# Kernel optimization log

Hardware: AMD Instinct MI355X
Metric: run time of the kernel (lower is better)

The kernel has to match this reference:

```python
import jax, jax.numpy as jnp
import numpy as np

DIM = 128          # per-stream channels (init arg `dim`)
C = 2 * DIM        # fused channels
NH = 8             # num_heads
HD = C // NH       # head_dim = 32
K = 3              # kernel_size
DIL = (2, 3)       # dilation list
ND = len(DIL)
SCALE = HD ** -0.5


def setup_inputs() -> dict:
    key = jax.random.key(0)
    ks = jax.random.split(key, 4)
    B, H, W = 4, 80, 80
    rgb = jax.random.normal(ks[0], (B, DIM, H, W), jnp.float32)
    ir = jax.random.normal(ks[1], (B, DIM, H, W), jnp.float32)
    w_qkv = jax.random.normal(ks[2], (3 * C, C), jnp.float32) * (C ** -0.5)
    w_proj = jax.random.normal(ks[3], (C, C), jnp.float32) * (C ** -0.5)
    b_proj = jnp.zeros((C,), jnp.float32)
    return {"rgb": rgb, "ir": ir, "w_qkv": w_qkv, "w_proj": w_proj, "b_proj": b_proj}


def _unfold(x, k, d):
    # nn.Unfold(k, dilation=d, padding=d*(k-1)//2, stride=1) -> [B, c, k*k, H, W]
    B, c, H, W = x.shape
    p = d * (k - 1) // 2
    xp = jnp.pad(x, ((0, 0), (0, 0), (p, p), (p, p)))
    pats = [xp[:, :, i * d:i * d + H, j * d:j * d + W]
            for i in range(k) for j in range(k)]
    return jnp.stack(pats, axis=2)


def _dilate_attention(q, k, v, d):
    # q,k,v: [B, c, H, W] with c = C // ND; attention over k*k dilated neighborhood
    B, c, H, W = q.shape
    h = c // HD
    N = H * W
    qr = q.reshape(B, h, HD, N)                      # [B,h,hd,N]
    ku = _unfold(k, K, d).reshape(B, h, HD, K * K, N)  # [B,h,hd,K2,N]
    vu = _unfold(v, K, d).reshape(B, h, HD, K * K, N)
    attn = jnp.einsum('bhdn,bhdkn->bhnk', qr, ku) * SCALE   # [B,h,N,K2]
    attn = jax.nn.softmax(attn, axis=-1)
    out = jnp.einsum('bhnk,bhdkn->bnhd', attn, vu)          # head-major channels
    return out.reshape(B, H, W, c)


def reference(rgb, ir, w_qkv, w_proj, b_proj):
    y = jnp.concatenate([rgb, ir], axis=1)            # [B, C, H, W]
    B, Cc, H, W = y.shape
    # 1x1 conv qkv, then split channels as [3, num_dilation, C//num_dilation]
    qkv = jnp.einsum('bchw,oc->bohw', y, w_qkv).reshape(B, 3, ND, Cc // ND, H, W)
    outs = [_dilate_attention(qkv[:, 0, i], qkv[:, 1, i], qkv[:, 2, i], DIL[i])
            for i in range(ND)]
    x = jnp.concatenate(outs, axis=-1)                # [B, H, W, C], dilation-major
    x = x @ w_proj.T + b_proj                         # proj Linear(C, C)
    # residual: add rgb to first half of channels, ir to second half
    return x + y.transpose(0, 2, 3, 1)
```

## Files before the change

kernel.cpp:

```cpp
#include <hip/hip_runtime.h>

#define HH 80
#define WW 80
#define NPIX 6400
#define NB 4
#define BN 25600
#define CDIM 256
#define QKVC 768
#define SCALE 0.17677669529663689f

typedef __attribute__((ext_vector_type(8))) short short8;
typedef __attribute__((ext_vector_type(4))) float floatx4;

__device__ __forceinline__ float b2f(ushort u) {
    return __uint_as_float(((uint)u) << 16);
}
__device__ __forceinline__ ushort f2b(float f) {
    uint u = __float_as_uint(f);
    return (ushort)((u + 0x7fffu + ((u >> 16) & 1u)) >> 16);
}
__device__ __forceinline__ void unpack8(uint4 v, float* f) {
    f[0] = __uint_as_float(v.x << 16); f[1] = __uint_as_float(v.x & 0xffff0000u);
    f[2] = __uint_as_float(v.y << 16); f[3] = __uint_as_float(v.y & 0xffff0000u);
    f[4] = __uint_as_float(v.z << 16); f[5] = __uint_as_float(v.z & 0xffff0000u);
    f[6] = __uint_as_float(v.w << 16); f[7] = __uint_as_float(v.w & 0xffff0000u);
}
__device__ __forceinline__ void gload_lds16(const void* gptr, void* lptr) {
    __builtin_amdgcn_global_load_lds(
        (const __attribute__((address_space(1))) unsigned int*)gptr,
        (__attribute__((address_space(3))) unsigned int*)lptr,
        16, 0, 0);
}

__global__ __launch_bounds__(256) void cast_w_k(
    const float* __restrict__ wq, const float* __restrict__ wp,
    ushort* __restrict__ wqb, ushort* __restrict__ wpb)
{
    int i = blockIdx.x * 256 + threadIdx.x;
    if (i < QKVC * CDIM) wqb[i] = f2b(wq[i]);
    if (i < CDIM * CDIM) wpb[i] = f2b(wp[i]);
}

__global__ __launch_bounds__(256) void cast_y_k(
    const float* __restrict__ rgb, const float* __restrict__ ir,
    ushort* __restrict__ Yb)
{
    __shared__ ushort T[32][72];
    const int tid = threadIdx.x;
    const int pix0 = blockIdx.x * 64;
    const int cb = blockIdx.y;
    const int b = blockIdx.z;

    const int pl = tid & 63, cg = tid >> 6;
    #pragma unroll
    for (int cc = 0; cc < 32; cc += 4) {
        int c = cb * 32 + cc + cg;
        const float* src = (c < 128) ? (rgb + ((size_t)b * 128 + c) * NPIX)
                                     : (ir + ((size_t)b * 128 + (c - 128)) * NPIX);
        T[cc + cg][pl] = f2b(src[pix0 + pl]);
    }
    __syncthreads();
    const int nl = tid >> 2, c0 = (tid & 3) * 8;
    ushort tmp[8];
    #pragma unroll
    for (int j = 0; j < 8; ++j) tmp[j] = T[c0 + j][nl];
    uint4 v;
    v.x = tmp[0] | ((uint)tmp[1] << 16);
    v.y = tmp[2] | ((uint)tmp[3] << 16);
    v.z = tmp[4] | ((uint)tmp[5] << 16);
    v.w = tmp[6] | ((uint)tmp[7] << 16);
    *(uint4*)(&Yb[((size_t)(b * NPIX + pix0 + nl)) * CDIM + cb * 32 + c0]) = v;
}

__global__ __launch_bounds__(256) void gemm_qkv_mfma(
    const ushort* __restrict__ Yb, const ushort* __restrict__ Wb,
    ushort* __restrict__ qkvb)
{
    __shared__ __align__(16) ushort As[128 * 40];
    __shared__ __align__(16) ushort Bs[128 * 40];
    const int tid = threadIdx.x;
    const int lane = tid & 63;
    const int wave = tid >> 6;
    const int wr = wave >> 1, wc = wave & 1;
    const int l15 = lane & 15, quad = lane >> 4;
    const int n0 = blockIdx.x * 128;
    const int o0 = blockIdx.y * 128;

    const int sm = tid >> 2;
    const int sk = (tid & 3) * 8;

    floatx4 acc[4][4] = {};

    for (int k0 = 0; k0 < CDIM; k0 += 32) {
        #pragma unroll
        for (int p = 0; p < 2; ++p) {
            int m = sm + p * 64;
            *(uint4*)(&As[m * 40 + sk]) =
                *(const uint4*)(&Yb[(size_t)(n0 + m) * CDIM + k0 + sk]);
            *(uint4*)(&Bs[m * 40 + sk]) =
                *(const uint4*)(&Wb[(size_t)(o0 + m) * CDIM + k0 + sk]);
        }
        __syncthreads();
        short8 af[4], bfr[4];
        #pragma unroll
        for (int i = 0; i < 4; ++i)
            af[i] = *(const short8*)(&As[(wr * 64 + i * 16 + l15) * 40 + quad * 8]);
        #pragma unroll
        for (int j = 0; j < 4; ++j)
            bfr[j] = *(const short8*)(&Bs[(wc * 64 + j * 16 + l15) * 40 + quad * 8]);
        #pragma unroll
        for (int i = 0; i < 4; ++i)
            #pragma unroll
            for (int j = 0; j < 4; ++j)
                acc[i][j] = __builtin_amdgcn_mfma_f32_16x16x32_bf16(
                    af[i], bfr[j], acc[i][j], 0, 0, 0);
        __syncthreads();
    }
    #pragma unroll
    for (int i = 0; i < 4; ++i)
        #pragma unroll
        for (int j = 0; j < 4; ++j)
            #pragma unroll
            for (int r = 0; r < 4; ++r) {
                int n = n0 + wr * 64 + i * 16 + quad * 4 + r;
                int o = o0 + wc * 64 + j * 16 + l15;
                qkvb[(size_t)n * QKVC + o] = f2b(acc[i][j][r]);
            }
}

template<int D>
__device__ __forceinline__ void attn_tile(
    const ushort* __restrict__ qkvb, ushort* __restrict__ Xb,
    ushort* kl, ushort* vl, int b, int dil_i, int head, int y0, int x0)
{
    constexpr int RW = 16 + 2 * D;
    constexpr int RP = RW * RW;
    const int tid = threadIdx.x;
    const int lane = tid & 63;
    const int wave = tid >> 6;
    const int obase = dil_i * 128 + head * 32;

    const int px = tid & 15, py = tid >> 4;
    const int n = b * NPIX + (y0 + py) * WW + (x0 + px);
    float q[32];
    {
        const uint4* qp = (const uint4*)(qkvb + (size_t)n * QKVC + obase);
        uint4 v0 = qp[0], v1 = qp[1], v2 = qp[2], v3 = qp[3];
        unpack8(v0, q); unpack8(v1, q + 8); unpack8(v2, q + 16); unpack8(v3, q + 24);
    }

    for (int p0 = 0; p0 < RP; p0 += 64) {
        int p = p0 + lane;
        int ry = p / RW, rx = p % RW;
        int gy = min(max(y0 - D + ry, 0), HH - 1);
        int gx = min(max(x0 - D + rx, 0), WW - 1);
        const ushort* row = qkvb + (size_t)(b * NPIX + gy * WW + gx) * QKVC + obase + wave * 8;
        if (p < RP) {
            gload_lds16(row + 256, kl + (size_t)(wave * RP + p0) * 8);
            gload_lds16(row + 512, vl + (size_t)(wave * RP + p0) * 8);
        }
    }
    __syncthreads();

    float sc[9];
    #pragma unroll
    for (int t = 0; t < 9; ++t) {
        const int dy = t / 3 - 1, dx = t % 3 - 1;
        const int yy = y0 + py + dy * D, xx = x0 + px + dx * D;
        const int p = (py + D + dy * D) * RW + (px + D + dx * D);
        float s = 0.f;
        if (yy >= 0 && yy < HH && xx >= 0 && xx < WW) {
            #pragma unroll
            for (int c = 0; c < 4; ++c) {
                float kv[8];
                unpack8(*(const uint4*)(kl + (size_t)(c * RP + p) * 8), kv);
                #pragma unroll
                for (int j = 0; j < 8; ++j) s += q[c * 8 + j] * kv[j];
            }
        }
        sc[t] = s * SCALE;
    }
    float m = sc[0];
    #pragma unroll
    for (int t = 1; t < 9; ++t) m = fmaxf(m, sc[t]);
    float sum = 0.f;
    #pragma unroll
    for (int t = 0; t < 9; ++t) { sc[t] = __expf(sc[t] - m); sum += sc[t]; }
    const float inv = 1.f / sum;

    float o[32];
    #pragma unroll
    for (int hd = 0; hd < 32; ++hd) o[hd] = 0.f;
    #pragma unroll
    for (int t = 0; t < 9; ++t) {
        const int dy = t / 3 - 1, dx = t % 3 - 1;
        const int yy = y0 + py + dy * D, xx = x0 + px + dx * D;
        const int p = (py + D + dy * D) * RW + (px + D + dx * D);
        if (yy >= 0 && yy < HH && xx >= 0 && xx < WW) {
            const float wgt = sc[t] * inv;
            #pragma unroll
            for (int c = 0; c < 4; ++c) {
                float vv[8];
                unpack8(*(const uint4*)(vl + (size_t)(c * RP + p) * 8), vv);
                #pragma unroll
                for (int j = 0; j < 8; ++j) o[c * 8 + j] += wgt * vv[j];
            }
        }
    }
    uint4* xp = (uint4*)(Xb + (size_t)n * CDIM + obase);
    #pragma unroll
    for (int m4 = 0; m4 < 4; ++m4) {
        uint4 v;
        v.x = f2b(o[8 * m4 + 0]) | ((uint)f2b(o[8 * m4 + 1]) << 16);
        v.y = f2b(o[8 * m4 + 2]) | ((uint)f2b(o[8 * m4 + 3]) << 16);
        v.z = f2b(o[8 * m4 + 4]) | ((uint)f2b(o[8 * m4 + 5]) << 16);
        v.w = f2b(o[8 * m4 + 6]) | ((uint)f2b(o[8 * m4 + 7]) << 16);
        xp[m4] = v;
    }
}

__global__ __launch_bounds__(256, 2) void attn2_k(
    const ushort* __restrict__ qkvb, ushort* __restrict__ Xb)
{
    __shared__ __align__(16) ushort kl[4 * 484 * 8];
    __shared__ __align__(16) ushort vl[4 * 484 * 8];
    const int tile = blockIdx.x;
    const int y0 = (tile / 5) * 16, x0 = (tile % 5) * 16;
    const int dh = blockIdx.y;
    const int b = blockIdx.z;
    const int dil_i = dh >> 2, head = dh & 3;
    if (dil_i == 0) attn_tile<2>(qkvb, Xb, kl, vl, b, 0, head, y0, x0);
    else            attn_tile<3>(qkvb, Xb, kl, vl, b, 1, head, y0, x0);
}

__global__ __launch_bounds__(256) void proj_mfma(
    const ushort* __restrict__ Xb, const ushort* __restrict__ Wpb,
    const float* __restrict__ bp, const ushort* __restrict__ Yb,
    float* __restrict__ out)
{
    __shared__ __align__(16) ushort As[128 * 40];
    __shared__ __align__(16) ushort Bs[128 * 40];
    const int tid = threadIdx.x;
    const int lane = tid & 63;
    const int wave = tid >> 6;
    const int wr = wave >> 1, wc = wave & 1;
    const int l15 = lane & 15, quad = lane >> 4;
    const int n0 = blockIdx.x * 128;
    const int o0 = blockIdx.y * 128;

    const int sm = tid >> 2;
    const int sk = (tid & 3) * 8;

    floatx4 acc[4][4] = {};

    for (int k0 = 0; k0 < CDIM; k0 += 32) {
        #pragma unroll
        for (int p = 0; p < 2; ++p) {
            int m = sm + p * 64;
            *(uint4*)(&As[m * 40 + sk]) =
                *(const uint4*)(&Xb[(size_t)(n0 + m) * CDIM + k0 + sk]);
            *(uint4*)(&Bs[m * 40 + sk]) =
                *(const uint4*)(&Wpb[(size_t)(o0 + m) * CDIM + k0 + sk]);
        }
        __syncthreads();
        short8 af[4], bfr[4];
        #pragma unroll
        for (int i = 0; i < 4; ++i)
            af[i] = *(const short8*)(&As[(wr * 64 + i * 16 + l15) * 40 + quad * 8]);
        #pragma unroll
        for (int j = 0; j < 4; ++j)
            bfr[j] = *(const short8*)(&Bs[(wc * 64 + j * 16 + l15) * 40 + quad * 8]);
        #pragma unroll
        for (int i = 0; i < 4; ++i)
            #pragma unroll
            for (int j = 0; j < 4; ++j)
                acc[i][j] = __builtin_amdgcn_mfma_f32_16x16x32_bf16(
                    af[i], bfr[j], acc[i][j], 0, 0, 0);
        __syncthreads();
    }
    #pragma unroll
    for (int i = 0; i < 4; ++i)
        #pragma unroll
        for (int j = 0; j < 4; ++j) {
            int o = o0 + wc * 64 + j * 16 + l15;
            float bias = bp[o];
            #pragma unroll
            for (int r = 0; r < 4; ++r) {
                int n = n0 + wr * 64 + i * 16 + quad * 4 + r;
                out[(size_t)n * CDIM + o] =
                    acc[i][j][r] + bias + b2f(Yb[(size_t)n * CDIM + o]);
            }
        }
}

extern "C" void kernel_launch(void* const* d_in, const int* in_sizes, int n_in,
                              void* d_out, int out_size, void* d_ws, size_t ws_size,
                              hipStream_t stream) {
    const float* rgb    = (const float*)d_in[0];
    const float* ir     = (const float*)d_in[1];
    const float* w_qkv  = (const float*)d_in[2];
    const float* w_proj = (const float*)d_in[3];
    const float* b_proj = (const float*)d_in[4];
    float* out = (float*)d_out;

    ushort* qkvb = (ushort*)d_ws;
    ushort* Yb   = qkvb + (size_t)BN * QKVC;
    ushort* Xb   = Yb + (size_t)BN * CDIM;
    ushort* Wqb  = Xb + (size_t)BN * CDIM;
    ushort* Wpb  = Wqb + (size_t)QKVC * CDIM;

    cast_w_k<<<QKVC, 256, 0, stream>>>(w_qkv, w_proj, Wqb, Wpb);
    cast_y_k<<<dim3(NPIX / 64, CDIM / 32, NB), 256, 0, stream>>>(rgb, ir, Yb);
    gemm_qkv_mfma<<<dim3(BN / 128, QKVC / 128), 256, 0, stream>>>(Yb, Wqb, qkvb);
    attn2_k<<<dim3(25, 8, NB), 256, 0, stream>>>(qkvb, Xb);
    proj_mfma<<<dim3(BN / 128, CDIM / 128), 256, 0, stream>>>(Xb, Wpb, b_proj, Yb, out);
}
```

Before: 158.0 us.

## Use direct global-to-LDS loads in GEMMs and reuse one LDS buffer for K and V

Both MFMA GEMMs now stage A and W tiles with global-to-LDS direct loads into an unpadded 32-wide layout, replacing register round-trip stores into a 40-wide padded layout. The attention kernel keeps a single LDS buffer: K is loaded and scored first, then V overwrites the same buffer after a barrier. This halves attention LDS use and drops the occupancy hint, aiming for more resident blocks. The trade-offs are a serialized V load after scoring, possible LDS bank conflicts without padding, and an extra barrier.

Result: faster. 149.9 us (-5.1%).

```diff
diff --git a/kernel.cpp b/kernel.cpp
--- a/kernel.cpp
+++ b/kernel.cpp
@@ -72,12 +72,51 @@
     *(uint4*)(&Yb[((size_t)(b * NPIX + pix0 + nl)) * CDIM + cb * 32 + c0]) = v;
 }
 
+__device__ __forceinline__ void gemm_nt_body(
+    const ushort* __restrict__ A, const ushort* __restrict__ W,
+    ushort* As, ushort* Bs, int n0, int o0, floatx4 acc[4][4])
+{
+    const int tid = threadIdx.x;
+    const int lane = tid & 63;
+    const int wave = tid >> 6;
+    const int wr = wave >> 1, wc = wave & 1;
+    const int l15 = lane & 15, quad = lane >> 4;
+
+    const int srow = tid >> 2;
+    const int sk   = (tid & 3) * 8;
+
+    for (int k0 = 0; k0 < CDIM; k0 += 32) {
+        #pragma unroll
+        for (int p = 0; p < 2; ++p) {
+            gload_lds16(&A[(size_t)(n0 + p * 64 + srow) * CDIM + k0 + sk],
+                        As + wave * 512 + p * 2048);
+            gload_lds16(&W[(size_t)(o0 + p * 64 + srow) * CDIM + k0 + sk],
+                        Bs + wave * 512 + p * 2048);
+        }
+        __syncthreads();
+        short8 af[4], bfr[4];
+        #pragma unroll
+        for (int i = 0; i < 4; ++i)
+            af[i] = *(const short8*)(&As[(wr * 64 + i * 16 + l15) * 32 + quad * 8]);
+        #pragma unroll
+        for (int j = 0; j < 4; ++j)
+            bfr[j] = *(const short8*)(&Bs[(wc * 64 + j * 16 + l15) * 32 + quad * 8]);
+        #pragma unroll
+        for (int i = 0; i < 4; ++i)
+            #pragma unroll
+            for (int j = 0; j < 4; ++j)
+                acc[i][j] = __builtin_amdgcn_mfma_f32_16x16x32_bf16(
+                    af[i], bfr[j], acc[i][j], 0, 0, 0);
+        __syncthreads();
+    }
+}
+
 __global__ __launch_bounds__(256) void gemm_qkv_mfma(
     const ushort* __restrict__ Yb, const ushort* __restrict__ Wb,
     ushort* __restrict__ qkvb)
 {
-    __shared__ __align__(16) ushort As[128 * 40];
-    __shared__ __align__(16) ushort Bs[128 * 40];
+    __shared__ __align__(16) ushort As[128 * 32];
+    __shared__ __align__(16) ushort Bs[128 * 32];
     const int tid = threadIdx.x;
     const int lane = tid & 63;
     const int wave = tid >> 6;
@@ -86,36 +125,9 @@
     const int n0 = blockIdx.x * 128;
     const int o0 = blockIdx.y * 128;
 
-    const int sm = tid >> 2;
-    const int sk = (tid & 3) * 8;
-
     floatx4 acc[4][4] = {};
-
-    for (int k0 = 0; k0 < CDIM; k0 += 32) {
-        #pragma unroll
-        for (int p = 0; p < 2; ++p) {
-            int m = sm + p * 64;
-            *(uint4*)(&As[m * 40 + sk]) =
-                *(const uint4*)(&Yb[(size_t)(n0 + m) * CDIM + k0 + sk]);
-            *(uint4*)(&Bs[m * 40 + sk]) =
-                *(const uint4*)(&Wb[(size_t)(o0 + m) * CDIM + k0 + sk]);
-        }
-        __syncthreads();
-        short8 af[4], bfr[4];
-        #pragma unroll
-        for (int i = 0; i < 4; ++i)
-            af[i] = *(const short8*)(&As[(wr * 64 + i * 16 + l15) * 40 + quad * 8]);
-        #pragma unroll
-        for (int j = 0; j < 4; ++j)
-            bfr[j] = *(const short8*)(&Bs[(wc * 64 + j * 16 + l15) * 40 + quad * 8]);
-        #pragma unroll
-        for (int i = 0; i < 4; ++i)
-            #pragma unroll
-            for (int j = 0; j < 4; ++j)
-                acc[i][j] = __builtin_amdgcn_mfma_f32_16x16x32_bf16(
-                    af[i], bfr[j], acc[i][j], 0, 0, 0);
-        __syncthreads();
-    }
+    gemm_nt_body(Yb, Wb, As, Bs, n0, o0, acc);
+
     #pragma unroll
     for (int i = 0; i < 4; ++i)
         #pragma unroll
@@ -131,7 +143,7 @@
 template<int D>
 __device__ __forceinline__ void attn_tile(
     const ushort* __restrict__ qkvb, ushort* __restrict__ Xb,
-    ushort* kl, ushort* vl, int b, int dil_i, int head, int y0, int x0)
+    ushort* kl, int b, int dil_i, int head, int y0, int x0)
 {
     constexpr int RW = 16 + 2 * D;
     constexpr int RP = RW * RW;
@@ -155,10 +167,8 @@
         int gy = min(max(y0 - D + ry, 0), HH - 1);
         int gx = min(max(x0 - D + rx, 0), WW - 1);
         const ushort* row = qkvb + (size_t)(b * NPIX + gy * WW + gx) * QKVC + obase + wave * 8;
-        if (p < RP) {
+        if (p < RP)
             gload_lds16(row + 256, kl + (size_t)(wave * RP + p0) * 8);
-            gload_lds16(row + 512, vl + (size_t)(wave * RP + p0) * 8);
-        }
     }
     __syncthreads();
 
@@ -188,6 +198,18 @@
     for (int t = 0; t < 9; ++t) { sc[t] = __expf(sc[t] - m); sum += sc[t]; }
     const float inv = 1.f / sum;
 
+    __syncthreads();
+    for (int p0 = 0; p0 < RP; p0 += 64) {
+        int p = p0 + lane;
+        int ry = p / RW, rx = p % RW;
+        int gy = min(max(y0 - D + ry, 0), HH - 1);
+        int gx = min(max(x0 - D + rx, 0), WW - 1);
+        const ushort* row = qkvb + (size_t)(b * NPIX + gy * WW + gx) * QKVC + obase + wave * 8;
+        if (p < RP)
+            gload_lds16(row + 512, kl + (size_t)(wave * RP + p0) * 8);
+    }
+    __syncthreads();
+
     float o[32];
     #pragma unroll
     for (int hd = 0; hd < 32; ++hd) o[hd] = 0.f;
@@ -201,7 +223,7 @@
             #pragma unroll
             for (int c = 0; c < 4; ++c) {
                 float vv[8];
-                unpack8(*(const uint4*)(vl + (size_t)(c * RP + p) * 8), vv);
+                unpack8(*(const uint4*)(kl + (size_t)(c * RP + p) * 8), vv);
                 #pragma unroll
                 for (int j = 0; j < 8; ++j) o[c * 8 + j] += wgt * vv[j];
             }
@@ -219,18 +241,17 @@
     }
 }
 
-__global__ __launch_bounds__(256, 2) void attn2_k(
+__global__ __launch_bounds__(256) void attn2_k(
     const ushort* __restrict__ qkvb, ushort* __restrict__ Xb)
 {
     __shared__ __align__(16) ushort kl[4 * 484 * 8];
-    __shared__ __align__(16) ushort vl[4 * 484 * 8];
     const int tile = blockIdx.x;
     const int y0 = (tile / 5) * 16, x0 = (tile % 5) * 16;
     const int dh = blockIdx.y;
     const int b = blockIdx.z;
     const int dil_i = dh >> 2, head = dh & 3;
-    if (dil_i == 0) attn_tile<2>(qkvb, Xb, kl, vl, b, 0, head, y0, x0);
-    else            attn_tile<3>(qkvb, Xb, kl, vl, b, 1, head, y0, x0);
+    if (dil_i == 0) attn_tile<2>(qkvb, Xb, kl, b, 0, head, y0, x0);
+    else            attn_tile<3>(qkvb, Xb, kl, b, 1, head, y0, x0);
 }
 
 __global__ __launch_bounds__(256) void proj_mfma(
@@ -238,8 +259,8 @@
     const float* __restrict__ bp, const ushort* __restrict__ Yb,
     float* __restrict__ out)
 {
-    __shared__ __align__(16) ushort As[128 * 40];
-    __shared__ __align__(16) ushort Bs[128 * 40];
+    __shared__ __align__(16) ushort As[128 * 32];
+    __shared__ __align__(16) ushort Bs[128 * 32];
     const int tid = threadIdx.x;
     const int lane = tid & 63;
     const int wave = tid >> 6;
@@ -248,36 +269,9 @@
     const int n0 = blockIdx.x * 128;
     const int o0 = blockIdx.y * 128;
 
-    const int sm = tid >> 2;
-    const int sk = (tid & 3) * 8;
-
     floatx4 acc[4][4] = {};
-
-    for (int k0 = 0; k0 < CDIM; k0 += 32) {
-        #pragma unroll
-        for (int p = 0; p < 2; ++p) {
-            int m = sm + p * 64;
-            *(uint4*)(&As[m * 40 + sk]) =
-                *(const uint4*)(&Xb[(size_t)(n0 + m) * CDIM + k0 + sk]);
-            *(uint4*)(&Bs[m * 40 + sk]) =
-                *(const uint4*)(&Wpb[(size_t)(o0 + m) * CDIM + k0 + sk]);
-        }
-        __syncthreads();
-        short8 af[4], bfr[4];
-        #pragma unroll
-        for (int i = 0; i < 4; ++i)
-            af[i] = *(const short8*)(&As[(wr * 64 + i * 16 + l15) * 40 + quad * 8]);
-        #pragma unroll
-        for (int j = 0; j < 4; ++j)
-            bfr[j] = *(const short8*)(&Bs[(wc * 64 + j * 16 + l15) * 40 + quad * 8]);
-        #pragma unroll
-        for (int i = 0; i < 4; ++i)
-            #pragma unroll
-            for (int j = 0; j < 4; ++j)
-                acc[i][j] = __builtin_amdgcn_mfma_f32_16x16x32_bf16(
-                    af[i], bfr[j], acc[i][j], 0, 0, 0);
-        __syncthreads();
-    }
+    gemm_nt_body(Xb, Wpb, As, Bs, n0, o0, acc);
+
     #pragma unroll
     for (int i = 0; i < 4; ++i)
         #pragma unroll
```
